# Performance work log

Measured on AMD Instinct MI355X. Metric: run time of the kernel, lower is better.

Reference implementation:

```python
import jax, jax.numpy as jnp
import numpy as np

N_NODES = 50000
N_EDGES = 600000
N_GRAPHS = 64
D_IN = 128
D_HID = 128
D_LAT = 64
BN_EPS = 1e-5


def setup_inputs() -> dict:
    key = jax.random.key(0)
    ks = jax.random.split(key, 8)
    x = jax.random.normal(ks[0], (N_NODES, D_IN), dtype=jnp.float32)
    edge_index = jax.random.randint(ks[1], (2, N_EDGES), 0, N_NODES, dtype=jnp.int64 if jax.config.jax_enable_x64 else jnp.int32)
    batch = jnp.sort(jax.random.randint(ks[2], (N_NODES,), 0, N_GRAPHS))
    d_cat = 13 * D_IN  # x + (mean,max,min,std) x (identity,amp,att)
    s = 1.0 / np.sqrt(d_cat)
    W0 = jax.random.normal(ks[3], (d_cat, D_HID), dtype=jnp.float32) * s
    W1 = jax.random.normal(ks[4], (13 * D_HID, D_HID), dtype=jnp.float32) * s
    W2 = jax.random.normal(ks[5], (13 * D_HID, D_HID), dtype=jnp.float32) * s
    fcW = jax.random.normal(ks[6], (D_HID, D_LAT), dtype=jnp.float32) * (1.0 / np.sqrt(D_HID))
    return {
        "x": x, "edge_index": edge_index, "batch": batch,
        "W0": W0, "b0": jnp.zeros((D_HID,), jnp.float32),
        "W1": W1, "b1": jnp.zeros((D_HID,), jnp.float32),
        "W2": W2, "b2": jnp.zeros((D_HID,), jnp.float32),
        "bn_gamma": jnp.ones((D_HID,), jnp.float32),
        "bn_beta": jnp.zeros((D_HID,), jnp.float32),
        "fcW": fcW, "fcb": jnp.zeros((D_LAT,), jnp.float32),
    }


def _pna_conv(h, W, b, src, dst, deg, delta):
    # h: [N, d]; messages gathered from source nodes per edge: [E, d]
    m = h[src]
    cnt = jnp.maximum(deg, 1.0)[:, None]
    ssum = jax.ops.segment_sum(m, dst, num_segments=N_NODES)
    mean = ssum / cnt
    ssq = jax.ops.segment_sum(m * m, dst, num_segments=N_NODES)
    std = jnp.sqrt(jnp.maximum(ssq / cnt - mean * mean, 0.0) + 1e-5)
    mx = jax.ops.segment_max(m, dst, num_segments=N_NODES)
    mn = jax.ops.segment_min(m, dst, num_segments=N_NODES)
    has = (deg > 0)[:, None]
    mx = jnp.where(has, mx, 0.0)
    mn = jnp.where(has, mn, 0.0)
    agg = jnp.concatenate([mean, mx, mn, std], axis=-1)  # [N, 4d]
    logd = jnp.log(deg + 1.0)[:, None]
    amp = logd / delta
    att = delta / jnp.maximum(logd, 1e-5)
    feat = jnp.concatenate([h, agg, agg * amp, agg * att], axis=-1)  # [N, 13d]
    return feat @ W + b


def reference(x, edge_index, batch, W0, b0, W1, b1, W2, b2, bn_gamma, bn_beta, fcW, fcb):
    src, dst = edge_index[0], edge_index[1]
    deg = jax.ops.segment_sum(jnp.ones((src.shape[0],), x.dtype), dst, num_segments=N_NODES)
    delta = jnp.mean(jnp.log(deg + 1.0))  # avg log-degree normalizer
    h = jax.nn.relu(_pna_conv(x, W0, b0, src, dst, deg, delta))
    h = jax.nn.relu(_pna_conv(h, W1, b1, src, dst, deg, delta))
    h = jax.nn.relu(_pna_conv(h, W2, b2, src, dst, deg, delta))
    # dropout is identity in eval mode
    pooled = jax.ops.segment_sum(h, batch, num_segments=N_GRAPHS)  # global_add_pool
    mu = jnp.mean(pooled, axis=0)
    var = jnp.var(pooled, axis=0)
    bn = (pooled - mu) / jnp.sqrt(var + BN_EPS) * bn_gamma + bn_beta
    return bn @ fcW + fcb
```

## Files before the change

kernel.cpp:

```cpp
#include <hip/hip_runtime.h>
#include <cstdint>
#include <cstddef>

#define N_NODESC 50000
#define N_PAD    50048
#define N_EDGESC 600000
#define N_GRAPHSC 64
#define D_HIDC   128
#define D_LATC   64
#define D_GS     512
#define D_WROW   1664

typedef unsigned short u16;
typedef unsigned int   u32;

typedef _Float16 f16x8 __attribute__((ext_vector_type(8)));
typedef _Float16 f16x2 __attribute__((ext_vector_type(2)));
typedef __fp16   hh2   __attribute__((ext_vector_type(2)));
typedef float    f32x4 __attribute__((ext_vector_type(4)));
typedef float    f32x2 __attribute__((ext_vector_type(2)));

__device__ __forceinline__ u16 f2h(float f) {
    return __builtin_bit_cast(u16, (_Float16)f);
}
__device__ __forceinline__ float h2f(u16 u) {
    return (float)__builtin_bit_cast(_Float16, u);
}
__device__ __forceinline__ u32 pkrtz(float a, float b) {
    return __builtin_bit_cast(u32, __builtin_amdgcn_cvt_pkrtz(a, b));
}

__device__ __forceinline__ f32x2 pk_add(f32x2 a, f32x2 b) {
    f32x2 d;
    asm("v_pk_add_f32 %0, %1, %2" : "=v"(d) : "v"(a), "v"(b));
    return d;
}
__device__ __forceinline__ f32x2 pk_fma(f32x2 a, f32x2 b, f32x2 c) {
    f32x2 d;
    asm("v_pk_fma_f32 %0, %1, %2, %3" : "=v"(d) : "v"(a), "v"(b), "v"(c));
    return d;
}

__device__ __forceinline__ void gll16(void* lds, const void* g) {
    __builtin_amdgcn_global_load_lds(
        (const __attribute__((address_space(1))) void*)g,
        (__attribute__((address_space(3))) void*)lds, 16, 0, 0);
}

__global__ void __launch_bounds__(256) k_setup(
        const float* __restrict__ x, const float* __restrict__ W0,
        const float* __restrict__ W1, const float* __restrict__ W2,
        const int* __restrict__ batch,
        u16* __restrict__ h, u16* __restrict__ Wt,
        int* __restrict__ zero_base, int nz, int ZB, int* __restrict__ goff) {
    int b = blockIdx.x;
    int t = threadIdx.x;
    if (b < ZB) {
        int i = b * 256 + t;
        if (i < nz) zero_base[i] = 0;
        return;
    }
    b -= ZB;
    if (b < 12500) {
        int i = b * 256 + t;
        float2 v = ((const float2*)x)[i];
        ((u32*)h)[i] = (u32)f2h(v.x) | ((u32)f2h(v.y) << 16);
        return;
    }
    b -= 12500;
    if (b < 2496) {
        int which = b / 832;
        int i = (b % 832) * 256 + t;
        const float* W = (which == 0) ? W0 : (which == 1) ? W1 : W2;
        int k = i / D_HIDC, j = i % D_HIDC;
        Wt[(size_t)which * D_WROW * D_HIDC + (size_t)j * D_WROW + k] = f2h(W[i]);
        return;
    }
    int g = t;
    if (g <= N_GRAPHSC) {
        int lo = 0, hi = N_NODESC;
        while (lo < hi) {
            int mid = (lo + hi) >> 1;
            if (batch[mid] < g) lo = mid + 1; else hi = mid;
        }
        goff[g] = lo;
    }
}

__global__ void k_count(const int* __restrict__ dst, int* __restrict__ deg) {
    int e = blockIdx.x * 256 + threadIdx.x;
    if (e < N_EDGESC) atomicAdd(&deg[dst[e]], 1);
}

__global__ void __launch_bounds__(256) k_scan_part(
        const int* __restrict__ deg, int* __restrict__ bsum,
        float* __restrict__ lsum) {
    __shared__ int s[256];
    __shared__ float ls[256];
    int idx = blockIdx.x * 256 + threadIdx.x;
    int v = (idx < N_NODESC) ? deg[idx] : 0;
    s[threadIdx.x] = v;
    ls[threadIdx.x] = (idx < N_NODESC) ? logf((float)v + 1.0f) : 0.0f;
    __syncthreads();
    for (int o = 128; o > 0; o >>= 1) {
        if (threadIdx.x < o) {
            s[threadIdx.x] += s[threadIdx.x + o];
            ls[threadIdx.x] += ls[threadIdx.x + o];
        }
        __syncthreads();
    }
    if (threadIdx.x == 0) { bsum[blockIdx.x] = s[0]; lsum[blockIdx.x] = ls[0]; }
}

__global__ void __launch_bounds__(256) k_scan_block(
        int* __restrict__ bsum, const float* __restrict__ lsum,
        float* __restrict__ delta_p) {
    __shared__ int s[256];
    __shared__ float ls[256];
    int t = threadIdx.x;
    int v = (t < 196) ? bsum[t] : 0;
    s[t] = v;
    ls[t] = (t < 196) ? lsum[t] : 0.0f;
    __syncthreads();
    for (int o = 1; o < 256; o <<= 1) {
        int add = (t >= o) ? s[t - o] : 0;
        __syncthreads();
        s[t] += add;
        __syncthreads();
    }
    if (t < 196) bsum[t] = s[t] - v;
    for (int o = 128; o > 0; o >>= 1) {
        if (t < o) ls[t] += ls[t + o];
        __syncthreads();
    }
    if (t == 0) delta_p[0] = ls[0] * (1.0f / (float)N_NODESC);
}

__global__ void __launch_bounds__(256) k_scan_final(
        const int* __restrict__ deg, const int* __restrict__ bsum,
        int* __restrict__ row_off) {
    __shared__ int s[256];
    int t = threadIdx.x;
    int idx = blockIdx.x * 256 + t;
    int v = (idx < N_NODESC) ? deg[idx] : 0;
    s[t] = v; __syncthreads();
    for (int o = 1; o < 256; o <<= 1) {
        int add = (t >= o) ? s[t - o] : 0;
        __syncthreads();
        s[t] += add;
        __syncthreads();
    }
    int excl = s[t] - v + bsum[blockIdx.x];
    if (idx < N_NODESC) row_off[idx] = excl;
    if (idx == 0) row_off[N_NODESC] = N_EDGESC;
}

__global__ void k_fill_csr(const int* __restrict__ src, const int* __restrict__ dst,
                           const int* __restrict__ row_off, int* __restrict__ cursor,
                           int* __restrict__ csr_src) {
    int e = blockIdx.x * 256 + threadIdx.x;
    if (e < N_EDGESC) {
        int d = dst[e];
        int pos = row_off[d] + atomicAdd(&cursor[d], 1);
        csr_src[pos] = src[e] << 8;
    }
}


__global__ void __launch_bounds__(256) k_aggregate(
        const u16* __restrict__ h, const int* __restrict__ row_off,
        const int* __restrict__ csr_src, u16* __restrict__ G) {
    int lane = threadIdx.x & 63;
    int half = lane >> 5, l32 = lane & 31;
    int n = blockIdx.x * 8 + ((threadIdx.x >> 6) << 1) + half;
    if (n >= N_NODESC) return;
    int c4 = 4 * l32;
    u32 c8 = 8u * (u32)l32;
    const char* h8 = (const char*)h;
    int beg = row_off[n], end = row_off[n + 1];
    const _Float16 NEG = (_Float16)(-65504.0f), POS = (_Float16)(65504.0f);
    f32x2 s01 = {0.f, 0.f}, s23 = {0.f, 0.f};
    f32x2 q01 = {0.f, 0.f}, q23 = {0.f, 0.f};
    f16x2 mx01 = {NEG, NEG}, mx23 = {NEG, NEG};
    f16x2 mn01 = {POS, POS}, mn23 = {POS, POS};

    #define PROC(u) { \
        f16x2 p01 = __builtin_bit_cast(f16x2, (u).x); \
        f16x2 p23 = __builtin_bit_cast(f16x2, (u).y); \
        f32x2 c01 = __builtin_convertvector(p01, f32x2); \
        f32x2 c23 = __builtin_convertvector(p23, f32x2); \
        s01 = pk_add(s01, c01); s23 = pk_add(s23, c23); \
        q01 = pk_fma(c01, c01, q01); q23 = pk_fma(c23, c23, q23); \
        mx01 = __builtin_elementwise_max(mx01, p01); \
        mx23 = __builtin_elementwise_max(mx23, p23); \
        mn01 = __builtin_elementwise_min(mn01, p01); \
        mn23 = __builtin_elementwise_min(mn23, p23); }

    int i = beg;
    for (; i + 3 < end; i += 4) {
        u32 e0 = (u32)csr_src[i],     e1 = (u32)csr_src[i + 1];
        u32 e2 = (u32)csr_src[i + 2], e3 = (u32)csr_src[i + 3];
        uint2 u0 = *(const uint2*)(h8 + (e0 + c8));
        uint2 u1 = *(const uint2*)(h8 + (e1 + c8));
        uint2 u2 = *(const uint2*)(h8 + (e2 + c8));
        uint2 u3 = *(const uint2*)(h8 + (e3 + c8));
        PROC(u0); PROC(u1); PROC(u2); PROC(u3);
    }
    for (; i < end; ++i) {
        u32 e0 = (u32)csr_src[i];
        uint2 u0 = *(const uint2*)(h8 + (e0 + c8));
        PROC(u0);
    }
    #undef PROC

    int d = end - beg;
    float inv = 1.0f / fmaxf((float)d, 1.0f);
    f32x2 vinv = {inv, inv};
    f32x2 me01 = s01 * vinv, me23 = s23 * vinv;
    f32x2 qn01 = q01 * vinv, qn23 = q23 * vinv;
    f32x2 var01 = qn01 - me01 * me01;
    f32x2 var23 = qn23 - me23 * me23;
    const f32x2 z2 = {0.f, 0.f};
    var01 = __builtin_elementwise_max(var01, z2);
    var23 = __builtin_elementwise_max(var23, z2);
    float sd0 = sqrtf(var01.x + 1e-5f), sd1 = sqrtf(var01.y + 1e-5f);
    float sd2 = sqrtf(var23.x + 1e-5f), sd3 = sqrtf(var23.y + 1e-5f);

    u32 mep01 = pkrtz(me01.x, me01.y), mep23 = pkrtz(me23.x, me23.y);
    u32 sdp01 = pkrtz(sd0, sd1),       sdp23 = pkrtz(sd2, sd3);
    u32 mxb01 = __builtin_bit_cast(u32, mx01), mxb23 = __builtin_bit_cast(u32, mx23);
    u32 mnb01 = __builtin_bit_cast(u32, mn01), mnb23 = __builtin_bit_cast(u32, mn23);
    if (d == 0) { mxb01 = mxb23 = mnb01 = mnb23 = 0u; }

    u16* base = G + (size_t)n * D_GS;
    uint2 M; M.x = mep01; M.y = mep23;
    uint2 X; X.x = mxb01; X.y = mxb23;
    uint2 N_; N_.x = mnb01; N_.y = mnb23;
    uint2 S; S.x = sdp01; S.y = sdp23;
    *(uint2*)(base + c4)       = M;
    *(uint2*)(base + 128 + c4) = X;
    *(uint2*)(base + 256 + c4) = N_;
    *(uint2*)(base + 384 + c4) = S;
}

__global__ void __launch_bounds__(256, 2) k_gemm(
        const u16* __restrict__ hin, const u16* __restrict__ G,
        const u16* __restrict__ Wt,
        const int* __restrict__ deg, const float* __restrict__ delta_p,
        const float* __restrict__ bias, u16* __restrict__ hout) {
    __shared__ _Float16 A1[128 * 64];
    __shared__ _Float16 A2[128 * 64];
    __shared__ _Float16 A3[128 * 64];
    __shared__ _Float16 Bt[128 * 64];
    const _Float16* Wf = (const _Float16*)Wt;
    const _Float16* Gf = (const _Float16*)G;
    const _Float16* Hf = (const _Float16*)hin;
    int n0 = blockIdx.x * 128;
    int t = threadIdx.x;
    int w = t >> 6, lane = t & 63;
    int srow8 = lane >> 3, sslot = lane & 7;
    int stg = (sslot ^ srow8) * 8;
    int q4 = lane >> 4, r16 = lane & 15;
    int sx0 = (q4 ^ (lane & 7)) * 8;
    int sx1 = ((q4 + 4) ^ (lane & 7)) * 8;
    int col = lane & 15;

    float delta = delta_p[0];
    float atv[8];
    _Float16 amh[8];
    #pragma unroll
    for (int nt = 0; nt < 8; nt++) {
        int node = n0 + nt * 16 + col;
        float logd = logf((float)deg[node] + 1.0f);
        amh[nt] = (_Float16)(logd / delta);
        atv[nt] = delta / fmaxf(logd, 1e-5f);
    }

    f32x4 acc[2][8], ac3[2][8];
    #pragma unroll
    for (int a = 0; a < 2; a++)
        #pragma unroll
        for (int b = 0; b < 8; b++) {
            acc[a][b] = (f32x4){0.f, 0.f, 0.f, 0.f};
            ac3[a][b] = (f32x4){0.f, 0.f, 0.f, 0.f};
        }

    for (int ki = 0; ki < 10; ki++) {
        int k0 = ki * 64;
        bool sreg = (k0 >= 128);
        __syncthreads();
        #pragma unroll
        for (int r = 0; r < 4; r++) {
            int rr = r * 4 + w;
            const _Float16* wrow = Wf + (size_t)(rr * 8 + srow8) * D_WROW;
            gll16(&A1[rr * 512], wrow + k0 + stg);
        }
        if (sreg) {
            #pragma unroll
            for (int r = 0; r < 4; r++) {
                int rr = r * 4 + w;
                const _Float16* wrow = Wf + (size_t)(rr * 8 + srow8) * D_WROW;
                gll16(&A2[rr * 512], wrow + 512 + k0 + stg);
                gll16(&A3[rr * 512], wrow + 1024 + k0 + stg);
            }
        }
        #pragma unroll
        for (int q = 0; q < 4; q++) {
            int rr = q * 4 + w;
            int row = n0 + rr * 8 + srow8;
            const _Float16* bsrc = (!sreg)
                ? Hf + (size_t)row * D_HIDC + k0 + stg
                : Gf + (size_t)row * D_GS + (k0 - 128) + stg;
            gll16(&Bt[rr * 512], bsrc);
        }
        __syncthreads();
        f16x8 a00 = *(const f16x8*)&A1[(w * 32 + r16) * 64 + sx0];
        f16x8 a01 = *(const f16x8*)&A1[(w * 32 + r16) * 64 + sx1];
        f16x8 a10 = *(const f16x8*)&A1[(w * 32 + 16 + r16) * 64 + sx0];
        f16x8 a11 = *(const f16x8*)&A1[(w * 32 + 16 + r16) * 64 + sx1];
        if (!sreg) {
            #pragma unroll
            for (int nt = 0; nt < 8; nt++) {
                f16x8 b0 = *(const f16x8*)&Bt[(nt * 16 + r16) * 64 + sx0];
                f16x8 b1 = *(const f16x8*)&Bt[(nt * 16 + r16) * 64 + sx1];
                acc[0][nt] = __builtin_amdgcn_mfma_f32_16x16x32_f16(a00, b0, acc[0][nt], 0, 0, 0);
                acc[1][nt] = __builtin_amdgcn_mfma_f32_16x16x32_f16(a10, b0, acc[1][nt], 0, 0, 0);
                acc[0][nt] = __builtin_amdgcn_mfma_f32_16x16x32_f16(a01, b1, acc[0][nt], 0, 0, 0);
                acc[1][nt] = __builtin_amdgcn_mfma_f32_16x16x32_f16(a11, b1, acc[1][nt], 0, 0, 0);
            }
        } else {
            f16x8 w2a0 = *(const f16x8*)&A2[(w * 32 + r16) * 64 + sx0];
            f16x8 w2a1 = *(const f16x8*)&A2[(w * 32 + r16) * 64 + sx1];
            f16x8 w2b0 = *(const f16x8*)&A2[(w * 32 + 16 + r16) * 64 + sx0];
            f16x8 w2b1 = *(const f16x8*)&A2[(w * 32 + 16 + r16) * 64 + sx1];
            f16x8 w3a0 = *(const f16x8*)&A3[(w * 32 + r16) * 64 + sx0];
            f16x8 w3a1 = *(const f16x8*)&A3[(w * 32 + r16) * 64 + sx1];
            f16x8 w3b0 = *(const f16x8*)&A3[(w * 32 + 16 + r16) * 64 + sx0];
            f16x8 w3b1 = *(const f16x8*)&A3[(w * 32 + 16 + r16) * 64 + sx1];
            #pragma unroll
            for (int nt = 0; nt < 8; nt++) {
                f16x8 b0 = *(const f16x8*)&Bt[(nt * 16 + r16) * 64 + sx0];
                f16x8 b1 = *(const f16x8*)&Bt[(nt * 16 + r16) * 64 + sx1];
                f16x8 bm0 = b0 * amh[nt];
                f16x8 bm1 = b1 * amh[nt];
                acc[0][nt] = __builtin_amdgcn_mfma_f32_16x16x32_f16(a00, b0, acc[0][nt], 0, 0, 0);
                acc[1][nt] = __builtin_amdgcn_mfma_f32_16x16x32_f16(a10, b0, acc[1][nt], 0, 0, 0);
                acc[0][nt] = __builtin_amdgcn_mfma_f32_16x16x32_f16(a01, b1, acc[0][nt], 0, 0, 0);
                acc[1][nt] = __builtin_amdgcn_mfma_f32_16x16x32_f16(a11, b1, acc[1][nt], 0, 0, 0);
                acc[0][nt] = __builtin_amdgcn_mfma_f32_16x16x32_f16(w2a0, bm0, acc[0][nt], 0, 0, 0);
                acc[1][nt] = __builtin_amdgcn_mfma_f32_16x16x32_f16(w2b0, bm0, acc[1][nt], 0, 0, 0);
                acc[0][nt] = __builtin_amdgcn_mfma_f32_16x16x32_f16(w2a1, bm1, acc[0][nt], 0, 0, 0);
                acc[1][nt] = __builtin_amdgcn_mfma_f32_16x16x32_f16(w2b1, bm1, acc[1][nt], 0, 0, 0);
                ac3[0][nt] = __builtin_amdgcn_mfma_f32_16x16x32_f16(w3a0, b0, ac3[0][nt], 0, 0, 0);
                ac3[1][nt] = __builtin_amdgcn_mfma_f32_16x16x32_f16(w3b0, b0, ac3[1][nt], 0, 0, 0);
                ac3[0][nt] = __builtin_amdgcn_mfma_f32_16x16x32_f16(w3a1, b1, ac3[0][nt], 0, 0, 0);
                ac3[1][nt] = __builtin_amdgcn_mfma_f32_16x16x32_f16(w3b1, b1, ac3[1][nt], 0, 0, 0);
            }
        }
    }
    int rowq = q4 * 4;
    #pragma unroll
    for (int nt = 0; nt < 8; nt++) {
        int node = n0 + nt * 16 + col;
        float at = atv[nt];
        #pragma unroll
        for (int mt = 0; mt < 2; mt++) {
            int jb = w * 32 + mt * 16 + rowq;
            f32x4 v = acc[mt][nt], v3 = ac3[mt][nt];
            ushort4 o;
            o.x = f2h(fmaxf(v.x + at * v3.x + bias[jb], 0.0f));
            o.y = f2h(fmaxf(v.y + at * v3.y + bias[jb + 1], 0.0f));
            o.z = f2h(fmaxf(v.z + at * v3.z + bias[jb + 2], 0.0f));
            o.w = f2h(fmaxf(v.w + at * v3.w + bias[jb + 3], 0.0f));
            *(ushort4*)&hout[(size_t)node * D_HIDC + jb] = o;
        }
    }
}


__global__ void __launch_bounds__(256) k_pool(
        const u16* __restrict__ h, const int* __restrict__ goff,
        float* __restrict__ pooled) {
    __shared__ float sm[256];
    int g = blockIdx.x >> 2, s = blockIdx.x & 3;
    int gb = goff[g], ge = goff[g + 1];
    int len = ge - gb;
    int q = (len + 3) >> 2;
    int nb = gb + s * q;
    int ne = min(nb + q, ge);
    int t = threadIdx.x;
    int j = t & 127, half = t >> 7;
    float acc = 0.0f;
    for (int n = nb + half; n < ne; n += 2)
        acc += h2f(h[(size_t)n * D_HIDC + j]);
    sm[t] = acc; __syncthreads();
    if (t < 128) {
        float v = sm[t] + sm[t + 128];
        atomicAdd(&pooled[g * D_HIDC + j], v);
    }
}

__global__ void __launch_bounds__(128) k_bn_fc(
        const float* __restrict__ pooled, const float* __restrict__ gamma,
        const float* __restrict__ beta, const float* __restrict__ fcW,
        const float* __restrict__ fcb, float* __restrict__ out) {
    __shared__ float bn[D_HIDC];
    int g = blockIdx.x, t = threadIdx.x;
    float s = 0.f, q = 0.f;
    for (int gg = 0; gg < N_GRAPHSC; gg++) {
        float v = pooled[gg * D_HIDC + t];
        s += v; q += v * v;
    }
    float mu = s * (1.0f / N_GRAPHSC);
    float var = q * (1.0f / N_GRAPHSC) - mu * mu;
    float inv = 1.0f / sqrtf(var + 1e-5f);
    bn[t] = (pooled[g * D_HIDC + t] - mu) * inv * gamma[t] + beta[t];
    __syncthreads();
    if (t < D_LATC) {
        float accum = fcb[t];
        for (int j = 0; j < D_HIDC; j++) accum += bn[j] * fcW[j * D_LATC + t];
        out[g * D_LATC + t] = accum;
    }
}


extern "C" void kernel_launch(void* const* d_in, const int* in_sizes, int n_in,
                              void* d_out, int out_size, void* d_ws, size_t ws_size,
                              hipStream_t stream) {
    const float* x     = (const float*)d_in[0];
    const int*   ei    = (const int*)d_in[1];
    const int*   batch = (const int*)d_in[2];
    const float* W0 = (const float*)d_in[3];
    const float* b0 = (const float*)d_in[4];
    const float* W1 = (const float*)d_in[5];
    const float* b1 = (const float*)d_in[6];
    const float* W2 = (const float*)d_in[7];
    const float* b2 = (const float*)d_in[8];
    const float* gamma = (const float*)d_in[9];
    const float* beta  = (const float*)d_in[10];
    const float* fcW   = (const float*)d_in[11];
    const float* fcb   = (const float*)d_in[12];
    float* out = (float*)d_out;
    const int* srcv = ei;
    const int* dstv = ei + N_EDGESC;

    char* p = (char*)d_ws;
    auto alloc = [&](size_t bytes) -> char* {
        char* r = p;
        p += (bytes + 255) & ~(size_t)255;
        return r;
    };
    int*   deg_cnt = (int*)alloc((size_t)N_PAD * 4);
    int*   cursor  = (int*)alloc((size_t)N_NODESC * 4);
    float* delta_p = (float*)alloc(4);
    float* pooled  = (float*)alloc((size_t)N_GRAPHSC * D_HIDC * 4);
    char*  zero_end = p;
    int*   row_off = (int*)alloc((size_t)(N_NODESC + 1) * 4);
    int*   goff    = (int*)alloc((size_t)(N_GRAPHSC + 1) * 4);
    int*   bsum    = (int*)alloc(256 * 4);
    float* lsum    = (float*)alloc(256 * 4);
    int*   csr_src = (int*)alloc((size_t)N_EDGESC * 4);
    u16*   Wt      = (u16*)alloc((size_t)3 * D_WROW * D_HIDC * 2);
    u16*   hA      = (u16*)alloc((size_t)N_PAD * D_HIDC * 2);
    u16*   hB      = (u16*)alloc((size_t)N_PAD * D_HIDC * 2);
    u16*   G       = (u16*)alloc((size_t)N_PAD * D_GS * 2);

    int nz = (int)((zero_end - (char*)deg_cnt) / 4);
    int ZB = (nz + 255) / 256;
    int setup_grid = ZB + 12500 + 2496 + 1;
    k_setup<<<setup_grid, 256, 0, stream>>>(x, W0, W1, W2, batch,
                                            hB, Wt, deg_cnt, nz, ZB, goff);
    k_count<<<(N_EDGESC + 255) / 256, 256, 0, stream>>>(dstv, deg_cnt);
    k_scan_part<<<196, 256, 0, stream>>>(deg_cnt, bsum, lsum);
    k_scan_block<<<1, 256, 0, stream>>>(bsum, lsum, delta_p);
    k_scan_final<<<196, 256, 0, stream>>>(deg_cnt, bsum, row_off);
    k_fill_csr<<<(N_EDGESC + 255) / 256, 256, 0, stream>>>(srcv, dstv, row_off, cursor, csr_src);

    const float* bs[3] = {b0, b1, b2};
    const u16* h_in[3]  = {hB, hA, hB};
    u16*       h_out[3] = {hA, hB, hA};
    size_t wsz = (size_t)D_WROW * D_HIDC;
    for (int l = 0; l < 3; l++) {
        k_aggregate<<<(N_NODESC + 7) / 8, 256, 0, stream>>>(
            h_in[l], row_off, csr_src, G);
        k_gemm<<<N_PAD / 128, 256, 0, stream>>>(
            h_in[l], G, Wt + (size_t)l * wsz, deg_cnt, delta_p, bs[l], h_out[l]);
    }
    k_pool<<<4 * N_GRAPHSC, 256, 0, stream>>>(h_out[2], goff, pooled);
    k_bn_fc<<<N_GRAPHSC, 128, 0, stream>>>(pooled, gamma, beta, fcW, fcb, out);
}
```

Baseline: 386.9 us.

## Tile weight transpose through LDS and software-pipeline edge index loads in aggregation

The weight transpose in the setup kernel now stages 64x128 tiles in shared memory and writes each transposed row as 16-byte vector stores, replacing scattered 2-byte strided writes. The aggregation loop is unrolled by 8, and the next batch of CSR source indices is loaded while the current gathers are being processed, to hide index-load latency. The cost is higher register use in the aggregation kernel and 16KB of static shared memory on every setup block, which may reduce occupancy for the other setup branches.

```diff
diff --git a/kernel.cpp b/kernel.cpp
--- a/kernel.cpp
+++ b/kernel.cpp
@@ -16,7 +16,6 @@
 
 typedef _Float16 f16x8 __attribute__((ext_vector_type(8)));
 typedef _Float16 f16x2 __attribute__((ext_vector_type(2)));
-typedef __fp16   hh2   __attribute__((ext_vector_type(2)));
 typedef float    f32x4 __attribute__((ext_vector_type(4)));
 typedef float    f32x2 __attribute__((ext_vector_type(2)));
 
@@ -53,6 +52,7 @@
         const int* __restrict__ batch,
         u16* __restrict__ h, u16* __restrict__ Wt,
         int* __restrict__ zero_base, int nz, int ZB, int* __restrict__ goff) {
+    __shared__ u16 lt[64 * 128];
     int b = blockIdx.x;
     int t = threadIdx.x;
     if (b < ZB) {
@@ -68,12 +68,27 @@
         return;
     }
     b -= 12500;
-    if (b < 2496) {
-        int which = b / 832;
-        int i = (b % 832) * 256 + t;
+    if (b < 78) {
+        int which = b / 26;
+        int k0 = (b % 26) * 64;
         const float* W = (which == 0) ? W0 : (which == 1) ? W1 : W2;
-        int k = i / D_HIDC, j = i % D_HIDC;
-        Wt[(size_t)which * D_WROW * D_HIDC + (size_t)j * D_WROW + k] = f2h(W[i]);
+        const float* src = W + (size_t)k0 * D_HIDC;
+        for (int i = t; i < 64 * 128; i += 256)
+            lt[i] = f2h(src[i]);
+        __syncthreads();
+        int j = t & 127, kh = t >> 7;
+        u16* dst = Wt + (size_t)which * D_WROW * D_HIDC
+                      + (size_t)j * D_WROW + k0 + kh * 32;
+        #pragma unroll
+        for (int c = 0; c < 4; c++) {
+            int kb = kh * 32 + c * 8;
+            u32 p0 = (u32)lt[(kb + 0) * 128 + j] | ((u32)lt[(kb + 1) * 128 + j] << 16);
+            u32 p1 = (u32)lt[(kb + 2) * 128 + j] | ((u32)lt[(kb + 3) * 128 + j] << 16);
+            u32 p2 = (u32)lt[(kb + 4) * 128 + j] | ((u32)lt[(kb + 5) * 128 + j] << 16);
+            u32 p3 = (u32)lt[(kb + 6) * 128 + j] | ((u32)lt[(kb + 7) * 128 + j] << 16);
+            uint4 v; v.x = p0; v.y = p1; v.z = p2; v.w = p3;
+            *(uint4*)(dst + c * 8) = v;
+        }
         return;
     }
     int g = t;
@@ -195,23 +210,44 @@
         mx23 = __builtin_elementwise_max(mx23, p23); \
         mn01 = __builtin_elementwise_min(mn01, p01); \
         mn23 = __builtin_elementwise_min(mn23, p23); }
+    #define GTH(e) (*(const uint2*)(h8 + ((e) + c8)))
 
     int i = beg;
+    if (i + 8 <= end) {
+        u32 e0 = (u32)csr_src[i],     e1 = (u32)csr_src[i + 1];
+        u32 e2 = (u32)csr_src[i + 2], e3 = (u32)csr_src[i + 3];
+        u32 e4 = (u32)csr_src[i + 4], e5 = (u32)csr_src[i + 5];
+        u32 e6 = (u32)csr_src[i + 6], e7 = (u32)csr_src[i + 7];
+        while (i + 16 <= end) {
+            uint2 u0 = GTH(e0), u1 = GTH(e1), u2 = GTH(e2), u3 = GTH(e3);
+            uint2 u4 = GTH(e4), u5 = GTH(e5), u6 = GTH(e6), u7 = GTH(e7);
+            e0 = (u32)csr_src[i + 8];  e1 = (u32)csr_src[i + 9];
+            e2 = (u32)csr_src[i + 10]; e3 = (u32)csr_src[i + 11];
+            e4 = (u32)csr_src[i + 12]; e5 = (u32)csr_src[i + 13];
+            e6 = (u32)csr_src[i + 14]; e7 = (u32)csr_src[i + 15];
+            PROC(u0); PROC(u1); PROC(u2); PROC(u3);
+            PROC(u4); PROC(u5); PROC(u6); PROC(u7);
+            i += 8;
+        }
+        uint2 u0 = GTH(e0), u1 = GTH(e1), u2 = GTH(e2), u3 = GTH(e3);
+        uint2 u4 = GTH(e4), u5 = GTH(e5), u6 = GTH(e6), u7 = GTH(e7);
+        PROC(u0); PROC(u1); PROC(u2); PROC(u3);
+        PROC(u4); PROC(u5); PROC(u6); PROC(u7);
+        i += 8;
+    }
     for (; i + 3 < end; i += 4) {
         u32 e0 = (u32)csr_src[i],     e1 = (u32)csr_src[i + 1];
         u32 e2 = (u32)csr_src[i + 2], e3 = (u32)csr_src[i + 3];
-        uint2 u0 = *(const uint2*)(h8 + (e0 + c8));
-        uint2 u1 = *(const uint2*)(h8 + (e1 + c8));
-        uint2 u2 = *(const uint2*)(h8 + (e2 + c8));
-        uint2 u3 = *(const uint2*)(h8 + (e3 + c8));
+        uint2 u0 = GTH(e0), u1 = GTH(e1), u2 = GTH(e2), u3 = GTH(e3);
         PROC(u0); PROC(u1); PROC(u2); PROC(u3);
     }
     for (; i < end; ++i) {
         u32 e0 = (u32)csr_src[i];
-        uint2 u0 = *(const uint2*)(h8 + (e0 + c8));
+        uint2 u0 = GTH(e0);
         PROC(u0);
     }
     #undef PROC
+    #undef GTH
 
     int d = end - beg;
     float inv = 1.0f / fmaxf((float)d, 1.0f);
@@ -467,7 +503,7 @@
 
     int nz = (int)((zero_end - (char*)deg_cnt) / 4);
     int ZB = (nz + 255) / 256;
-    int setup_grid = ZB + 12500 + 2496 + 1;
+    int setup_grid = ZB + 12500 + 78 + 1;
     k_setup<<<setup_grid, 256, 0, stream>>>(x, W0, W1, W2, batch,
                                             hB, Wt, deg_cnt, nz, ZB, goff);
     k_count<<<(N_EDGESC + 255) / 256, 256, 0, stream>>>(dstv, deg_cnt);
```

After: 378.5 us. 1.02x faster.
